# Optimization experiments

Hardware: AMD Instinct MI355X
Metric: run time of the kernel (lower is better)

Reference implementation:

```python
import jax, jax.numpy as jnp
import numpy as np

KH, KW = 3, 3
N = KH * KW  # kernel points

def _grid_offset(H, W_):
    # Faithful to TF code: stack(meshgrid(ij)) -> (2,kh,kw) -> reshape(-1,2)
    ii, jj = jnp.meshgrid(jnp.arange(KH), jnp.arange(KW), indexing='ij')
    init_off = jnp.stack([ii, jj]).reshape(-1, 2).astype(jnp.float32)  # (N,2)
    ph, pw = (KH - 1) // 2, (KW - 1) // 2
    gi, gj = jnp.meshgrid(jnp.arange(-ph, H - ph), jnp.arange(-pw, W_ - pw), indexing='ij')
    grid = jnp.stack([gi, gj], axis=-1).astype(jnp.float32)[:, :, None, :]  # (H,W,1,2)
    return grid + init_off  # (H,W,N,2)

def setup_inputs() -> dict:
    key = jax.random.key(0)
    k1, k2, k3 = jax.random.split(key, 3)
    B, H, W_, C, Cout = 8, 128, 128, 32, 32
    x = jax.random.normal(k1, (B, H, W_, C), dtype=jnp.float32)
    offsets = jax.random.normal(k2, (B, H, W_, 2 * N), dtype=jnp.float32)
    W = jax.random.normal(k3, (N, C, Cout), dtype=jnp.float32) * 0.02
    b = jnp.zeros((Cout,), dtype=jnp.float32)
    return {"x": x, "offsets": offsets, "W": W, "b": b}

def reference(x, offsets, W, b):
    B, H, W_, C = x.shape
    grid_offset = _grid_offset(H, W_)  # (H,W,N,2)
    coords = grid_offset[None] + offsets.reshape(B, H, W_, N, 2)  # (B,H,W,N,2)
    c0 = jnp.clip(coords[..., 0], 0.0, jnp.float32(H - 1))
    c1 = jnp.clip(coords[..., 1], 0.0, jnp.float32(W_ - 1))
    lt0 = jnp.floor(c0).astype(jnp.int32)
    lt1 = jnp.floor(c1).astype(jnp.int32)
    rb0 = jnp.ceil(c0).astype(jnp.int32)
    rb1 = jnp.ceil(c1).astype(jnp.int32)
    bidx = jnp.arange(B)[:, None, None, None]
    gather = lambda i, j: x[bidx, i, j]  # (B,H,W,N,C)
    v_lt = gather(lt0, lt1)
    v_rb = gather(rb0, rb1)
    v_lb = gather(lt0, rb1)
    v_rt = gather(rb0, lt1)
    f0 = (c0 - lt0.astype(jnp.float32))[..., None]
    f1 = (c1 - lt1.astype(jnp.float32))[..., None]
    v_t = v_lt + (v_rt - v_lt) * f0
    v_b = v_lb + (v_rb - v_lb) * f0
    mapped = v_t + (v_b - v_t) * f1  # (B,H,W,N,C)
    # conv3d with (1,1,N,C,Cout) VALID kernel == per-pixel contraction over (N,C)
    return jnp.einsum('bhwnc,nco->bhwo', mapped, W) + b
```

## Files before the change

### kernel.cpp

```cpp
#include <hip/hip_runtime.h>
#include <hip/hip_bf16.h>

typedef __bf16 bf16x8 __attribute__((ext_vector_type(8)));
typedef float f32x4 __attribute__((ext_vector_type(4)));

#define NB 8
#define NH 128
#define NWID 128
#define NC 32
#define NO 32
#define NPTS 9
#define KTOT 288
#define KPAD 296
#define PB 64

__global__ __launch_bounds__(256, 2)
void dcn_kernel(const float* __restrict__ x,
                const float* __restrict__ off,
                const float* __restrict__ Wsrc,
                const float* __restrict__ bias,
                float* __restrict__ out)
{
    __shared__ __hip_bfloat16 sMap[PB][KPAD];
    __shared__ __hip_bfloat16 sW[NO][KPAD];

    const int tid = threadIdx.x;

    for (int idx = tid; idx < NPTS * NC * NO; idx += 256) {
        int n = idx >> 10;
        int r = idx & 1023;
        int c = r >> 5;
        int o = r & 31;
        sW[o][(n << 5) + c] = __float2bfloat16(Wsrc[idx]);
    }

    const int pix0 = blockIdx.x * PB;

    {
        const int cg  = tid & 15;
        const int grp = tid >> 4;
        const int ioff0[9] = {0,0,1,2,2,1,0,2,1};
        const int ioff1[9] = {0,1,1,2,0,2,1,0,2};
        #pragma unroll
        for (int pp = 0; pp < 4; ++pp) {
            const int lp = grp + (pp << 4);
            const int gp = pix0 + lp;
            const int bidx = gp >> 14;
            const int hh = (gp >> 7) & 127;
            const int ww = gp & 127;
            const float* xb = x + ((size_t)bidx << 19);
            const float* offp = off + (size_t)gp * 18;
            #pragma unroll
            for (int n = 0; n < 9; ++n) {
                float o0 = offp[2 * n];
                float o1 = offp[2 * n + 1];
                float c0 = (float)(hh - 1 + ioff0[n]) + o0;
                float c1 = (float)(ww - 1 + ioff1[n]) + o1;
                c0 = fminf(fmaxf(c0, 0.f), 127.f);
                c1 = fminf(fmaxf(c1, 0.f), 127.f);
                float fl0 = floorf(c0), fl1 = floorf(c1);
                int lt0 = (int)fl0, lt1 = (int)fl1;
                int rb0 = (int)ceilf(c0), rb1 = (int)ceilf(c1);
                float f0 = c0 - fl0, f1 = c1 - fl1;
                const float2* r_lt = (const float2*)(xb + (size_t)((lt0 << 7) + lt1) * NC) + cg;
                const float2* r_rt = (const float2*)(xb + (size_t)((rb0 << 7) + lt1) * NC) + cg;
                const float2* r_lb = (const float2*)(xb + (size_t)((lt0 << 7) + rb1) * NC) + cg;
                const float2* r_rb = (const float2*)(xb + (size_t)((rb0 << 7) + rb1) * NC) + cg;
                float2 vlt = *r_lt;
                float2 vrt = *r_rt;
                float2 vlb = *r_lb;
                float2 vrb = *r_rb;
                float tx = vlt.x + (vrt.x - vlt.x) * f0;
                float ty = vlt.y + (vrt.y - vlt.y) * f0;
                float bx = vlb.x + (vrb.x - vlb.x) * f0;
                float by = vlb.y + (vrb.y - vlb.y) * f0;
                float mx = tx + (bx - tx) * f1;
                float my = ty + (by - ty) * f1;
                __hip_bfloat162 mp = __float22bfloat162_rn(make_float2(mx, my));
                *reinterpret_cast<__hip_bfloat162*>(&sMap[lp][(n << 5) + (cg << 1)]) = mp;
            }
        }
    }
    __syncthreads();

    {
        const int wave = tid >> 6;
        const int lane = tid & 63;
        const int mrow = (wave << 4) + (lane & 15);
        const int kq = (lane >> 4) << 3;
        f32x4 acc0 = {0.f, 0.f, 0.f, 0.f};
        f32x4 acc1 = {0.f, 0.f, 0.f, 0.f};
        #pragma unroll
        for (int ks = 0; ks < 9; ++ks) {
            const int k = (ks << 5) + kq;
            bf16x8 a  = *reinterpret_cast<const bf16x8*>(&sMap[mrow][k]);
            bf16x8 b0 = *reinterpret_cast<const bf16x8*>(&sW[lane & 15][k]);
            bf16x8 b1 = *reinterpret_cast<const bf16x8*>(&sW[(lane & 15) + 16][k]);
            acc0 = __builtin_amdgcn_mfma_f32_16x16x32_bf16(a, b0, acc0, 0, 0, 0);
            acc1 = __builtin_amdgcn_mfma_f32_16x16x32_bf16(a, b1, acc1, 0, 0, 0);
        }
        const int ocol = lane & 15;
        const float bias0 = bias[ocol];
        const float bias1 = bias[ocol + 16];
        const int rbase = (wave << 4) + ((lane >> 4) << 2);
        #pragma unroll
        for (int i = 0; i < 4; ++i) {
            const int gp = pix0 + rbase + i;
            float* op = out + (size_t)gp * NO;
            op[ocol]      = acc0[i] + bias0;
            op[ocol + 16] = acc1[i] + bias1;
        }
    }
}

extern "C" void kernel_launch(void* const* d_in, const int* in_sizes, int n_in,
                              void* d_out, int out_size, void* d_ws, size_t ws_size,
                              hipStream_t stream) {
    const float* x    = (const float*)d_in[0];
    const float* off  = (const float*)d_in[1];
    const float* Wsrc = (const float*)d_in[2];
    const float* bias = (const float*)d_in[3];
    float* out = (float*)d_out;
    const int npix = NB * NH * NWID;
    dcn_kernel<<<npix / PB, 256, 0, stream>>>(x, off, Wsrc, bias, out);
}
```

Before: 53.65 us.

## Fuse bilinear sampling directly into MFMA A-operand registers, drop shared staging

Each lane now computes the bilinear-interpolated values for the exact MFMA A-fragment it owns (one pixel, eight channels per kernel point), packs them to bf16 in registers and feeds the MFMA directly. This removes the sMap shared-memory buffer, its writes and reads, and part of the synchronisation. With less shared memory in use, the launch bound is raised to 4 blocks per CU. Gathers become 16-byte vector loads per corner instead of 8-byte loads. The cost is more register pressure per thread, and the gather latency now sits in the MFMA dependency chain.

```diff
diff --git a/kernel.cpp b/kernel.cpp
--- a/kernel.cpp
+++ b/kernel.cpp
@@ -10,18 +10,16 @@
 #define NC 32
 #define NO 32
 #define NPTS 9
-#define KTOT 288
 #define KPAD 296
 #define PB 64
 
-__global__ __launch_bounds__(256, 2)
+__global__ __launch_bounds__(256, 4)
 void dcn_kernel(const float* __restrict__ x,
                 const float* __restrict__ off,
                 const float* __restrict__ Wsrc,
                 const float* __restrict__ bias,
                 float* __restrict__ out)
 {
-    __shared__ __hip_bfloat16 sMap[PB][KPAD];
     __shared__ __hip_bfloat16 sW[NO][KPAD];
 
     const int tid = threadIdx.x;
@@ -33,83 +31,79 @@
         int o = r & 31;
         sW[o][(n << 5) + c] = __float2bfloat16(Wsrc[idx]);
     }
-
-    const int pix0 = blockIdx.x * PB;
-
-    {
-        const int cg  = tid & 15;
-        const int grp = tid >> 4;
-        const int ioff0[9] = {0,0,1,2,2,1,0,2,1};
-        const int ioff1[9] = {0,1,1,2,0,2,1,0,2};
-        #pragma unroll
-        for (int pp = 0; pp < 4; ++pp) {
-            const int lp = grp + (pp << 4);
-            const int gp = pix0 + lp;
-            const int bidx = gp >> 14;
-            const int hh = (gp >> 7) & 127;
-            const int ww = gp & 127;
-            const float* xb = x + ((size_t)bidx << 19);
-            const float* offp = off + (size_t)gp * 18;
-            #pragma unroll
-            for (int n = 0; n < 9; ++n) {
-                float o0 = offp[2 * n];
-                float o1 = offp[2 * n + 1];
-                float c0 = (float)(hh - 1 + ioff0[n]) + o0;
-                float c1 = (float)(ww - 1 + ioff1[n]) + o1;
-                c0 = fminf(fmaxf(c0, 0.f), 127.f);
-                c1 = fminf(fmaxf(c1, 0.f), 127.f);
-                float fl0 = floorf(c0), fl1 = floorf(c1);
-                int lt0 = (int)fl0, lt1 = (int)fl1;
-                int rb0 = (int)ceilf(c0), rb1 = (int)ceilf(c1);
-                float f0 = c0 - fl0, f1 = c1 - fl1;
-                const float2* r_lt = (const float2*)(xb + (size_t)((lt0 << 7) + lt1) * NC) + cg;
-                const float2* r_rt = (const float2*)(xb + (size_t)((rb0 << 7) + lt1) * NC) + cg;
-                const float2* r_lb = (const float2*)(xb + (size_t)((lt0 << 7) + rb1) * NC) + cg;
-                const float2* r_rb = (const float2*)(xb + (size_t)((rb0 << 7) + rb1) * NC) + cg;
-                float2 vlt = *r_lt;
-                float2 vrt = *r_rt;
-                float2 vlb = *r_lb;
-                float2 vrb = *r_rb;
-                float tx = vlt.x + (vrt.x - vlt.x) * f0;
-                float ty = vlt.y + (vrt.y - vlt.y) * f0;
-                float bx = vlb.x + (vrb.x - vlb.x) * f0;
-                float by = vlb.y + (vrb.y - vlb.y) * f0;
-                float mx = tx + (bx - tx) * f1;
-                float my = ty + (by - ty) * f1;
-                __hip_bfloat162 mp = __float22bfloat162_rn(make_float2(mx, my));
-                *reinterpret_cast<__hip_bfloat162*>(&sMap[lp][(n << 5) + (cg << 1)]) = mp;
-            }
-        }
-    }
     __syncthreads();
 
-    {
-        const int wave = tid >> 6;
-        const int lane = tid & 63;
-        const int mrow = (wave << 4) + (lane & 15);
-        const int kq = (lane >> 4) << 3;
-        f32x4 acc0 = {0.f, 0.f, 0.f, 0.f};
-        f32x4 acc1 = {0.f, 0.f, 0.f, 0.f};
+    const int wave = tid >> 6;
+    const int lane = tid & 63;
+    const int row  = lane & 15;
+    const int cq   = lane >> 4;
+    const int pix0 = blockIdx.x * PB;
+    const int gp   = pix0 + (wave << 4) + row;
+    const int bidx = gp >> 14;
+    const int hh   = (gp >> 7) & 127;
+    const int ww   = gp & 127;
+    const float* xb = x + ((size_t)bidx << 19);
+    const float* xc = xb + (cq << 3);
+    const float* offp = off + (size_t)gp * 18;
+
+    const int ioff0[9] = {0,0,1,2,2,1,0,2,1};
+    const int ioff1[9] = {0,1,1,2,0,2,1,0,2};
+
+    float2 ov[9];
+    #pragma unroll
+    for (int n = 0; n < 9; ++n)
+        ov[n] = *reinterpret_cast<const float2*>(offp + 2 * n);
+
+    f32x4 acc0 = {0.f, 0.f, 0.f, 0.f};
+    f32x4 acc1 = {0.f, 0.f, 0.f, 0.f};
+
+    #pragma unroll
+    for (int n = 0; n < 9; ++n) {
+        float c0 = fminf(fmaxf((float)(hh - 1 + ioff0[n]) + ov[n].x, 0.f), 127.f);
+        float c1 = fminf(fmaxf((float)(ww - 1 + ioff1[n]) + ov[n].y, 0.f), 127.f);
+        float fl0 = floorf(c0), fl1 = floorf(c1);
+        int lt0 = (int)fl0, lt1 = (int)fl1;
+        int rb0 = (int)ceilf(c0), rb1 = (int)ceilf(c1);
+        float f0 = c0 - fl0, f1 = c1 - fl1;
+
+        const float* p_lt = xc + (((lt0 << 7) + lt1) << 5);
+        const float* p_rt = xc + (((rb0 << 7) + lt1) << 5);
+        const float* p_lb = xc + (((lt0 << 7) + rb1) << 5);
+        const float* p_rb = xc + (((rb0 << 7) + rb1) << 5);
+        f32x4 lt_a = *(const f32x4*)p_lt, lt_b = *(const f32x4*)(p_lt + 4);
+        f32x4 rt_a = *(const f32x4*)p_rt, rt_b = *(const f32x4*)(p_rt + 4);
+        f32x4 lb_a = *(const f32x4*)p_lb, lb_b = *(const f32x4*)(p_lb + 4);
+        f32x4 rb_a = *(const f32x4*)p_rb, rb_b = *(const f32x4*)(p_rb + 4);
+
+        union { bf16x8 v; __hip_bfloat16 h[8]; } au;
         #pragma unroll
-        for (int ks = 0; ks < 9; ++ks) {
-            const int k = (ks << 5) + kq;
-            bf16x8 a  = *reinterpret_cast<const bf16x8*>(&sMap[mrow][k]);
-            bf16x8 b0 = *reinterpret_cast<const bf16x8*>(&sW[lane & 15][k]);
-            bf16x8 b1 = *reinterpret_cast<const bf16x8*>(&sW[(lane & 15) + 16][k]);
-            acc0 = __builtin_amdgcn_mfma_f32_16x16x32_bf16(a, b0, acc0, 0, 0, 0);
-            acc1 = __builtin_amdgcn_mfma_f32_16x16x32_bf16(a, b1, acc1, 0, 0, 0);
+        for (int j = 0; j < 4; ++j) {
+            float t = lt_a[j] + (rt_a[j] - lt_a[j]) * f0;
+            float b = lb_a[j] + (rb_a[j] - lb_a[j]) * f0;
+            au.h[j] = __float2bfloat16(t + (b - t) * f1);
         }
-        const int ocol = lane & 15;
-        const float bias0 = bias[ocol];
-        const float bias1 = bias[ocol + 16];
-        const int rbase = (wave << 4) + ((lane >> 4) << 2);
         #pragma unroll
-        for (int i = 0; i < 4; ++i) {
-            const int gp = pix0 + rbase + i;
-            float* op = out + (size_t)gp * NO;
-            op[ocol]      = acc0[i] + bias0;
-            op[ocol + 16] = acc1[i] + bias1;
+        for (int j = 0; j < 4; ++j) {
+            float t = lt_b[j] + (rt_b[j] - lt_b[j]) * f0;
+            float b = lb_b[j] + (rb_b[j] - lb_b[j]) * f0;
+            au.h[4 + j] = __float2bfloat16(t + (b - t) * f1);
         }
+
+        const int kk = (n << 5) + (cq << 3);
+        bf16x8 b0 = *reinterpret_cast<const bf16x8*>(&sW[row][kk]);
+        bf16x8 b1 = *reinterpret_cast<const bf16x8*>(&sW[row + 16][kk]);
+        acc0 = __builtin_amdgcn_mfma_f32_16x16x32_bf16(au.v, b0, acc0, 0, 0, 0);
+        acc1 = __builtin_amdgcn_mfma_f32_16x16x32_bf16(au.v, b1, acc1, 0, 0, 0);
+    }
+
+    const float bias0 = bias[row];
+    const float bias1 = bias[row + 16];
+    const int rbase = (wave << 4) + (cq << 2);
+    #pragma unroll
+    for (int i = 0; i < 4; ++i) {
+        float* op = out + (size_t)(pix0 + rbase + i) * NO;
+        op[row]      = acc0[i] + bias0;
+        op[row + 16] = acc1[i] + bias1;
     }
 }
 
```

New measurement: 79.14 us. 47.5% more time.
